# Performance work log

Hardware: AMD Instinct MI355X
Metric: run time of the kernel (lower is better)

## Reference

```python
import jax, jax.numpy as jnp
import numpy as np

N = 40000      # nodes
E = 640000     # edges (avg degree 16)
IN = 128
H = 128
OUT = 64


def setup_inputs() -> dict:
    key = jax.random.key(0)
    ks = jax.random.split(key, 10)
    s_in = 1.0 / np.sqrt(IN)
    s_h = 1.0 / np.sqrt(H)
    return {
        "x": jax.random.normal(ks[0], (N, IN), jnp.float32),
        "edge_index": jax.random.randint(ks[1], (2, E), 0, N, dtype=jnp.int64),
        "W1l": jax.random.normal(ks[2], (IN, H), jnp.float32) * s_in,
        "W1r": jax.random.normal(ks[3], (IN, H), jnp.float32) * s_in,
        "b1": jnp.zeros((H,), jnp.float32),
        "W2l": jax.random.normal(ks[4], (H, H), jnp.float32) * s_h,
        "W2r": jax.random.normal(ks[5], (H, H), jnp.float32) * s_h,
        "b2": jnp.zeros((H,), jnp.float32),
        "Wout": jax.random.normal(ks[6], (H, OUT), jnp.float32) * s_h,
        "bout": jnp.zeros((OUT,), jnp.float32),
    }


def _sage_conv(x, src, dst, Wl, Wr, b):
    # mean aggregation of source features onto destination nodes
    msg = x[src]                                   # [E, d] gather
    agg = jax.ops.segment_sum(msg, dst, num_segments=N)       # [N, d]
    deg = jax.ops.segment_sum(jnp.ones((src.shape[0],), x.dtype), dst,
                              num_segments=N)                  # [N]
    agg = agg / jnp.maximum(deg, 1.0)[:, None]
    # PyG SAGEConv: lin_l(aggregated neighbors) + lin_r(root); bias on lin_l
    return agg @ Wl + x @ Wr + b


def reference(x, edge_index, W1l, W1r, b1, W2l, W2r, b2, Wout, bout):
    src, dst = edge_index[0], edge_index[1]
    h = jax.nn.relu(_sage_conv(x, src, dst, W1l, W1r, b1))
    h = jax.nn.relu(_sage_conv(h, src, dst, W2l, W2r, b2))
    return h @ Wout + bout
```

## Files before the change

### kernel.cpp

```cpp
#include <hip/hip_runtime.h>


typedef __attribute__((ext_vector_type(8))) short short8v;
typedef __attribute__((ext_vector_type(4))) float f32x4;
typedef __attribute__((ext_vector_type(4))) _Float16 half4v;
typedef __attribute__((ext_vector_type(8))) _Float16 half8v;

#define CAP 64

static __device__ __forceinline__ unsigned short f2bf(float f) {
  unsigned u = __float_as_uint(f);
  u += 0x7fffu + ((u >> 16) & 1u);
  return (unsigned short)(u >> 16);
}
static __device__ __forceinline__ float bf2f(unsigned short h) {
  return __uint_as_float(((unsigned)h) << 16);
}

__global__ __launch_bounds__(256) void k_setup(
    const int* __restrict__ src, const int* __restrict__ dst,
    int* __restrict__ cnt, ushort* __restrict__ csr,
    const float* __restrict__ W1l, const float* __restrict__ W1r,
    const float* __restrict__ W2l, const float* __restrict__ W2r,
    ushort* __restrict__ w1h, ushort* __restrict__ w1lo,
    ushort* __restrict__ w2h, ushort* __restrict__ w2lo,
    const float* __restrict__ Wout, ushort* __restrict__ woh,
    ushort* __restrict__ wol, const float* __restrict__ x,
    _Float16* __restrict__ xh, int E, int N) {
  int t = blockIdx.x * 256 + threadIdx.x;
  if (t < E) {
    int d = dst[t];
    int pos = atomicAdd(&cnt[d], 1);
    if (pos < CAP) csr[(size_t)d * CAP + pos] = (ushort)src[t];
    return;
  }
  t -= E;
  if (t < 8192) {
    const bool is2 = t >= 4096;
    int u = t & 4095;
    const float* Wl = is2 ? W2l : W1l;
    const float* Wr = is2 ? W2r : W1r;
    ushort* wh = is2 ? w2h : w1h;
    ushort* wlo = is2 ? w2lo : w1lo;
    int l = u & 63;
    int n = (u >> 6) & 7;
    int s = u >> 9;
    int col = n * 16 + (l & 15);
    int kb = s * 32 + ((l >> 4) * 8);
    size_t base = ((size_t)(s * 8 + n) * 64 + l) * 8;
#pragma unroll
    for (int j = 0; j < 8; ++j) {
      int k = kb + j;
      float w = (k < 128) ? Wl[(size_t)k * 128 + col] : Wr[(size_t)(k - 128) * 128 + col];
      unsigned short hb = f2bf(w);
      wh[base + j] = hb;
      wlo[base + j] = f2bf(w - bf2f(hb));
    }
    return;
  }
  t -= 8192;
  if (t < 1024) {
    int l = t & 63;
    int n = (t >> 6) & 3;
    int s = t >> 8;
    int col = n * 16 + (l & 15);
    int kb = s * 32 + ((l >> 4) * 8);
    size_t base = ((size_t)(s * 4 + n) * 64 + l) * 8;
#pragma unroll
    for (int j = 0; j < 8; ++j) {
      float w = Wout[(size_t)(kb + j) * 64 + col];
      unsigned short hb = f2bf(w);
      woh[base + j] = hb;
      wol[base + j] = f2bf(w - bf2f(hb));
    }
    return;
  }
  t -= 1024;
  if (t < N * 32) {
    float4 v = reinterpret_cast<const float4*>(x)[t];
    half4v o = {(_Float16)v.x, (_Float16)v.y, (_Float16)v.z, (_Float16)v.w};
    reinterpret_cast<half4v*>(xh)[t] = o;
  }
}

__global__ __launch_bounds__(256) void k_agg(const _Float16* __restrict__ feat,
                                             const int* __restrict__ cnt,
                                             const ushort* __restrict__ csr,
                                             _Float16* __restrict__ agg, int N) {
  const int lane = threadIdx.x & 63;
  const int q = lane >> 4;
  const int c = (lane & 15) * 8;
  const int wave = threadIdx.x >> 6;
  const int node0 = blockIdx.x * 16 + wave * 4 + q;
  const bool valid = node0 < N;
  const int node = valid ? node0 : (N - 1);
  const int deg = cnt[node];
  const int stored = deg < CAP ? deg : CAP;
  const ushort* idx = csr + (size_t)node * CAP;
  float a[8] = {};
  for (int j = 0; j < stored; j += 16) {
    half8v v[16];
#pragma unroll
    for (int u = 0; u < 16; ++u) {
      if (j + u < stored) {
        int nb = idx[j + u];
        v[u] = *reinterpret_cast<const half8v*>(feat + (size_t)nb * 128 + c);
      }
    }
#pragma unroll
    for (int t = 0; t < 8; ++t) {
      float s0 = 0.f, s1 = 0.f, s2 = 0.f, s3 = 0.f;
#pragma unroll
      for (int u = 0; u < 16; u += 4) {
        if (j + u + 0 < stored) s0 += (float)v[u + 0][t];
        if (j + u + 1 < stored) s1 += (float)v[u + 1][t];
        if (j + u + 2 < stored) s2 += (float)v[u + 2][t];
        if (j + u + 3 < stored) s3 += (float)v[u + 3][t];
      }
      a[t] += (s0 + s1) + (s2 + s3);
    }
  }
  if (valid) {
    float invd = 1.0f / fmaxf((float)deg, 1.0f);
    half8v o;
#pragma unroll
    for (int t = 0; t < 8; ++t) o[t] = (_Float16)(a[t] * invd);
    *reinterpret_cast<half8v*>(agg + (size_t)node * 128 + c) = o;
  }
}

__global__ __launch_bounds__(256) void k_gemm1(
    const _Float16* __restrict__ aggh, const _Float16* __restrict__ rooth,
    const ushort* __restrict__ wh, const ushort* __restrict__ wl_,
    const float* __restrict__ bias, _Float16* __restrict__ outh, int M) {
  const int lane = threadIdx.x & 63;
  const int wave = threadIdx.x >> 6;
  const int row = blockIdx.x * 64 + wave * 16;
  f32x4 acc[8] = {};

  for (int s = 0; s < 8; ++s) {
    const int kb = (s & 3) * 32;
    const size_t aoff = (size_t)(row + (lane & 15)) * 128 + kb + (lane >> 4) * 8;
    const _Float16* ap = (s < 4) ? (aggh + aoff) : (rooth + aoff);
    half8v hv = *reinterpret_cast<const half8v*>(ap);
    float av[8];
#pragma unroll
    for (int j = 0; j < 8; ++j) av[j] = (float)hv[j];
    short8v ah, al;
#pragma unroll
    for (int j = 0; j < 8; ++j) {
      unsigned short hb = f2bf(av[j]);
      ah[j] = (short)hb;
      al[j] = (short)f2bf(av[j] - bf2f(hb));
    }
    const size_t sbase = (size_t)s * 8 * 64 * 8 + (size_t)lane * 8;
#pragma unroll
    for (int n = 0; n < 8; ++n) {
      short8v bh = *reinterpret_cast<const short8v*>(wh + sbase + (size_t)n * 64 * 8);
      short8v bl = *reinterpret_cast<const short8v*>(wl_ + sbase + (size_t)n * 64 * 8);
      acc[n] = __builtin_amdgcn_mfma_f32_16x16x32_bf16(ah, bh, acc[n], 0, 0, 0);
      acc[n] = __builtin_amdgcn_mfma_f32_16x16x32_bf16(ah, bl, acc[n], 0, 0, 0);
      acc[n] = __builtin_amdgcn_mfma_f32_16x16x32_bf16(al, bh, acc[n], 0, 0, 0);
    }
  }

  const int r0 = row + (lane >> 4) * 4;
  const int col0 = lane & 15;
#pragma unroll
  for (int n = 0; n < 8; ++n) {
    int col = n * 16 + col0;
    float bv = bias[col];
#pragma unroll
    for (int r = 0; r < 4; ++r) {
      float v = fmaxf(acc[n][r] + bv, 0.f);
      outh[(size_t)(r0 + r) * 128 + col] = (_Float16)v;
    }
  }
}

__global__ __launch_bounds__(256) void k_gemm2_out(
    const _Float16* __restrict__ aggh, const _Float16* __restrict__ rooth,
    const ushort* __restrict__ w2h, const ushort* __restrict__ w2l,
    const float* __restrict__ b2, const ushort* __restrict__ woh,
    const ushort* __restrict__ wol, const float* __restrict__ bout,
    float* __restrict__ out, int M) {
  __shared__ float H[64][132];
  const int lane = threadIdx.x & 63;
  const int wave = threadIdx.x >> 6;
  const int row = blockIdx.x * 64 + wave * 16;
  f32x4 acc[8] = {};

  for (int s = 0; s < 8; ++s) {
    const int kb = (s & 3) * 32;
    const size_t aoff = (size_t)(row + (lane & 15)) * 128 + kb + (lane >> 4) * 8;
    const _Float16* ap = (s < 4) ? (aggh + aoff) : (rooth + aoff);
    half8v hv = *reinterpret_cast<const half8v*>(ap);
    float av[8];
#pragma unroll
    for (int j = 0; j < 8; ++j) av[j] = (float)hv[j];
    short8v ah, al;
#pragma unroll
    for (int j = 0; j < 8; ++j) {
      unsigned short hb = f2bf(av[j]);
      ah[j] = (short)hb;
      al[j] = (short)f2bf(av[j] - bf2f(hb));
    }
    const size_t sbase = (size_t)s * 8 * 64 * 8 + (size_t)lane * 8;
#pragma unroll
    for (int n = 0; n < 8; ++n) {
      short8v bh = *reinterpret_cast<const short8v*>(w2h + sbase + (size_t)n * 64 * 8);
      short8v bl = *reinterpret_cast<const short8v*>(w2l + sbase + (size_t)n * 64 * 8);
      acc[n] = __builtin_amdgcn_mfma_f32_16x16x32_bf16(ah, bh, acc[n], 0, 0, 0);
      acc[n] = __builtin_amdgcn_mfma_f32_16x16x32_bf16(ah, bl, acc[n], 0, 0, 0);
      acc[n] = __builtin_amdgcn_mfma_f32_16x16x32_bf16(al, bh, acc[n], 0, 0, 0);
    }
  }

  const int r0loc = wave * 16 + (lane >> 4) * 4;
  const int col0 = lane & 15;
#pragma unroll
  for (int n = 0; n < 8; ++n) {
    int col = n * 16 + col0;
    float bv = b2[col];
#pragma unroll
    for (int r = 0; r < 4; ++r) {
      H[r0loc + r][col] = fmaxf(acc[n][r] + bv, 0.f);
    }
  }
  __syncthreads();

  f32x4 acc2[4] = {};
  for (int s = 0; s < 4; ++s) {
    const float* hp = &H[wave * 16 + (lane & 15)][s * 32 + (lane >> 4) * 8];
    float av[8];
#pragma unroll
    for (int j = 0; j < 8; ++j) av[j] = hp[j];
    short8v ah, al;
#pragma unroll
    for (int j = 0; j < 8; ++j) {
      unsigned short hb = f2bf(av[j]);
      ah[j] = (short)hb;
      al[j] = (short)f2bf(av[j] - bf2f(hb));
    }
    const size_t sbase = (size_t)s * 4 * 64 * 8 + (size_t)lane * 8;
#pragma unroll
    for (int n = 0; n < 4; ++n) {
      short8v bh = *reinterpret_cast<const short8v*>(woh + sbase + (size_t)n * 64 * 8);
      short8v bl = *reinterpret_cast<const short8v*>(wol + sbase + (size_t)n * 64 * 8);
      acc2[n] = __builtin_amdgcn_mfma_f32_16x16x32_bf16(ah, bh, acc2[n], 0, 0, 0);
      acc2[n] = __builtin_amdgcn_mfma_f32_16x16x32_bf16(ah, bl, acc2[n], 0, 0, 0);
      acc2[n] = __builtin_amdgcn_mfma_f32_16x16x32_bf16(al, bh, acc2[n], 0, 0, 0);
    }
  }

  const int r0 = row + (lane >> 4) * 4;
#pragma unroll
  for (int n = 0; n < 4; ++n) {
    int col = n * 16 + col0;
    float bv = bout[col];
#pragma unroll
    for (int r = 0; r < 4; ++r) {
      out[(size_t)(r0 + r) * 64 + col] = acc2[n][r] + bv;
    }
  }
}

extern "C" void kernel_launch(void* const* d_in, const int* in_sizes, int n_in,
                              void* d_out, int out_size, void* d_ws, size_t ws_size,
                              hipStream_t stream) {
  const float* x    = (const float*)d_in[0];
  const int*   ei   = (const int*)d_in[1];
  const float* W1l  = (const float*)d_in[2];
  const float* W1r  = (const float*)d_in[3];
  const float* b1   = (const float*)d_in[4];
  const float* W2l  = (const float*)d_in[5];
  const float* W2r  = (const float*)d_in[6];
  const float* b2   = (const float*)d_in[7];
  const float* Wout = (const float*)d_in[8];
  const float* bout = (const float*)d_in[9];
  float* out = (float*)d_out;

  const int N = in_sizes[0] / 128;
  const int E = in_sizes[1] / 2;
  const int* src = ei;
  const int* dst = ei + E;

  auto align = [](size_t b) { return (b + 255) & ~(size_t)255; };
  char* p = (char*)d_ws;
  int* cnt       = (int*)p;       p += align((size_t)N * 4);
  ushort* csr    = (ushort*)p;    p += align((size_t)N * CAP * 2);
  _Float16* xh   = (_Float16*)p;  p += align((size_t)N * 128 * 2);
  _Float16* h1h  = (_Float16*)p;  p += align((size_t)N * 128 * 2);
  _Float16* aggh = (_Float16*)p;  p += align((size_t)N * 128 * 2);
  ushort* w1h    = (ushort*)p;    p += align(32768 * 2);
  ushort* w1lo   = (ushort*)p;    p += align(32768 * 2);
  ushort* w2h    = (ushort*)p;    p += align(32768 * 2);
  ushort* w2lo   = (ushort*)p;    p += align(32768 * 2);
  ushort* woh    = (ushort*)p;    p += align(8192 * 2);
  ushort* wol    = (ushort*)p;    p += align(8192 * 2);

  (void)hipMemsetAsync(cnt, 0, (size_t)N * 4, stream);

  const int gemmBlocks = (N + 63) / 64;
  const int aggBlocks = (N + 15) / 16;
  const int setupThreads = E + 8192 + 1024 + N * 32;

  k_setup<<<(setupThreads + 255) / 256, 256, 0, stream>>>(
      src, dst, cnt, csr, W1l, W1r, W2l, W2r, w1h, w1lo, w2h, w2lo,
      Wout, woh, wol, x, xh, E, N);

  k_agg<<<aggBlocks, 256, 0, stream>>>(xh, cnt, csr, aggh, N);
  k_gemm1<<<gemmBlocks, 256, 0, stream>>>(aggh, xh, w1h, w1lo, b1, h1h, N);

  k_agg<<<aggBlocks, 256, 0, stream>>>(h1h, cnt, csr, aggh, N);
  k_gemm2_out<<<gemmBlocks, 256, 0, stream>>>(aggh, h1h, w2h, w2lo, b2,
                                              woh, wol, bout, out, N);
}
```

Baseline: 155.5 us.

## Build compact CSR via count, prefix scan, and fill instead of fixed-cap buckets

Replaces the fixed 64-slot per-node neighbor buckets with an exact CSR: the setup kernel only counts in-degrees, then a three-kernel prefix scan builds row pointers and a fill pass scatters source indices with atomics. The aggregation kernel reads from the row pointers and its inner batch shrinks from 16 to 8 neighbors. The aim is to drop the degree cap (a correctness fix for high-degree nodes) and to give denser, contiguous index reads. In exchange it adds four extra launches, including a single-thread serial block scan, and a second pass of atomics over the edges.

```diff
diff --git a/kernel.cpp b/kernel.cpp
--- a/kernel.cpp
+++ b/kernel.cpp
@@ -6,8 +6,6 @@
 typedef __attribute__((ext_vector_type(4))) _Float16 half4v;
 typedef __attribute__((ext_vector_type(8))) _Float16 half8v;
 
-#define CAP 64
-
 static __device__ __forceinline__ unsigned short f2bf(float f) {
   unsigned u = __float_as_uint(f);
   u += 0x7fffu + ((u >> 16) & 1u);
@@ -18,8 +16,7 @@
 }
 
 __global__ __launch_bounds__(256) void k_setup(
-    const int* __restrict__ src, const int* __restrict__ dst,
-    int* __restrict__ cnt, ushort* __restrict__ csr,
+    const int* __restrict__ dst, int* __restrict__ cnt,
     const float* __restrict__ W1l, const float* __restrict__ W1r,
     const float* __restrict__ W2l, const float* __restrict__ W2r,
     ushort* __restrict__ w1h, ushort* __restrict__ w1lo,
@@ -29,9 +26,7 @@
     _Float16* __restrict__ xh, int E, int N) {
   int t = blockIdx.x * 256 + threadIdx.x;
   if (t < E) {
-    int d = dst[t];
-    int pos = atomicAdd(&cnt[d], 1);
-    if (pos < CAP) csr[(size_t)d * CAP + pos] = (ushort)src[t];
+    atomicAdd(&cnt[dst[t]], 1);
     return;
   }
   t -= E;
@@ -83,9 +78,84 @@
   }
 }
 
+__global__ __launch_bounds__(1024) void k_bsum(const int* __restrict__ cnt,
+                                               int* __restrict__ blockSums, int N) {
+  __shared__ int ws[16];
+  int i = blockIdx.x * 1024 + threadIdx.x;
+  int v = (i < N) ? cnt[i] : 0;
+#pragma unroll
+  for (int d = 32; d > 0; d >>= 1) v += __shfl_xor(v, d, 64);
+  if ((threadIdx.x & 63) == 0) ws[threadIdx.x >> 6] = v;
+  __syncthreads();
+  if (threadIdx.x == 0) {
+    int s = 0;
+#pragma unroll
+    for (int w = 0; w < 16; ++w) s += ws[w];
+    blockSums[blockIdx.x] = s;
+  }
+}
+
+__global__ __launch_bounds__(64) void k_bscan(const int* __restrict__ blockSums,
+                                              int* __restrict__ blockOff,
+                                              int* __restrict__ rowptr, int nb, int N) {
+  if (threadIdx.x == 0) {
+    int run = 0;
+    for (int i = 0; i < nb; ++i) {
+      blockOff[i] = run;
+      run += blockSums[i];
+    }
+    rowptr[N] = run;
+  }
+}
+
+__global__ __launch_bounds__(1024) void k_escan(const int* __restrict__ cnt,
+                                                const int* __restrict__ blockOff,
+                                                int* __restrict__ rowptr,
+                                                int* __restrict__ cursor, int N) {
+  __shared__ int warpSums[16];
+  const int tid = threadIdx.x;
+  const int lane = tid & 63, wid = tid >> 6;
+  int i = blockIdx.x * 1024 + tid;
+  int v = (i < N) ? cnt[i] : 0;
+  int s = v;
+#pragma unroll
+  for (int d = 1; d < 64; d <<= 1) {
+    int t = __shfl_up(s, d, 64);
+    if (lane >= d) s += t;
+  }
+  if (lane == 63) warpSums[wid] = s;
+  __syncthreads();
+  if (tid < 16) {
+    int w = warpSums[tid];
+#pragma unroll
+    for (int d = 1; d < 16; d <<= 1) {
+      int t = __shfl_up(w, d, 16);
+      if (tid >= d) w += t;
+    }
+    warpSums[tid] = w;
+  }
+  __syncthreads();
+  int ex = blockOff[blockIdx.x] + (wid ? warpSums[wid - 1] : 0) + s - v;
+  if (i < N) {
+    rowptr[i] = ex;
+    cursor[i] = ex;
+  }
+}
+
+__global__ __launch_bounds__(256) void k_fill(const int* __restrict__ src,
+                                              const int* __restrict__ dst,
+                                              int* __restrict__ cursor,
+                                              ushort* __restrict__ csr_src, int E) {
+  int e = blockIdx.x * 256 + threadIdx.x;
+  if (e < E) {
+    int pos = atomicAdd(&cursor[dst[e]], 1);
+    csr_src[pos] = (ushort)src[e];
+  }
+}
+
 __global__ __launch_bounds__(256) void k_agg(const _Float16* __restrict__ feat,
-                                             const int* __restrict__ cnt,
-                                             const ushort* __restrict__ csr,
+                                             const int* __restrict__ rowptr,
+                                             const ushort* __restrict__ csr_src,
                                              _Float16* __restrict__ agg, int N) {
   const int lane = threadIdx.x & 63;
   const int q = lane >> 4;
@@ -94,30 +164,32 @@
   const int node0 = blockIdx.x * 16 + wave * 4 + q;
   const bool valid = node0 < N;
   const int node = valid ? node0 : (N - 1);
-  const int deg = cnt[node];
-  const int stored = deg < CAP ? deg : CAP;
-  const ushort* idx = csr + (size_t)node * CAP;
+  const int beg = rowptr[node];
+  const int deg = rowptr[node + 1] - beg;
+  const ushort* idx = csr_src + beg;
   float a[8] = {};
-  for (int j = 0; j < stored; j += 16) {
-    half8v v[16];
-#pragma unroll
-    for (int u = 0; u < 16; ++u) {
-      if (j + u < stored) {
-        int nb = idx[j + u];
-        v[u] = *reinterpret_cast<const half8v*>(feat + (size_t)nb * 128 + c);
-      }
-    }
+  for (int j = 0; j < deg; j += 8) {
+    half8v v0, v1, v2, v3, v4, v5, v6, v7;
+    if (j + 0 < deg) { int nb = idx[j + 0]; v0 = *reinterpret_cast<const half8v*>(feat + (size_t)nb * 128 + c); }
+    if (j + 1 < deg) { int nb = idx[j + 1]; v1 = *reinterpret_cast<const half8v*>(feat + (size_t)nb * 128 + c); }
+    if (j + 2 < deg) { int nb = idx[j + 2]; v2 = *reinterpret_cast<const half8v*>(feat + (size_t)nb * 128 + c); }
+    if (j + 3 < deg) { int nb = idx[j + 3]; v3 = *reinterpret_cast<const half8v*>(feat + (size_t)nb * 128 + c); }
+    if (j + 4 < deg) { int nb = idx[j + 4]; v4 = *reinterpret_cast<const half8v*>(feat + (size_t)nb * 128 + c); }
+    if (j + 5 < deg) { int nb = idx[j + 5]; v5 = *reinterpret_cast<const half8v*>(feat + (size_t)nb * 128 + c); }
+    if (j + 6 < deg) { int nb = idx[j + 6]; v6 = *reinterpret_cast<const half8v*>(feat + (size_t)nb * 128 + c); }
+    if (j + 7 < deg) { int nb = idx[j + 7]; v7 = *reinterpret_cast<const half8v*>(feat + (size_t)nb * 128 + c); }
 #pragma unroll
     for (int t = 0; t < 8; ++t) {
-      float s0 = 0.f, s1 = 0.f, s2 = 0.f, s3 = 0.f;
-#pragma unroll
-      for (int u = 0; u < 16; u += 4) {
-        if (j + u + 0 < stored) s0 += (float)v[u + 0][t];
-        if (j + u + 1 < stored) s1 += (float)v[u + 1][t];
-        if (j + u + 2 < stored) s2 += (float)v[u + 2][t];
-        if (j + u + 3 < stored) s3 += (float)v[u + 3][t];
-      }
-      a[t] += (s0 + s1) + (s2 + s3);
+      float s0 = 0.f, s1 = 0.f;
+      if (j + 0 < deg) s0 += (float)v0[t];
+      if (j + 1 < deg) s1 += (float)v1[t];
+      if (j + 2 < deg) s0 += (float)v2[t];
+      if (j + 3 < deg) s1 += (float)v3[t];
+      if (j + 4 < deg) s0 += (float)v4[t];
+      if (j + 5 < deg) s1 += (float)v5[t];
+      if (j + 6 < deg) s0 += (float)v6[t];
+      if (j + 7 < deg) s1 += (float)v7[t];
+      a[t] += s0 + s1;
     }
   }
   if (valid) {
@@ -288,7 +360,11 @@
   auto align = [](size_t b) { return (b + 255) & ~(size_t)255; };
   char* p = (char*)d_ws;
   int* cnt       = (int*)p;       p += align((size_t)N * 4);
-  ushort* csr    = (ushort*)p;    p += align((size_t)N * CAP * 2);
+  int* rowptr    = (int*)p;       p += align((size_t)(N + 1) * 4);
+  int* cursor    = (int*)p;       p += align((size_t)N * 4);
+  int* blockSums = (int*)p;       p += align(64 * 4);
+  int* blockOff  = (int*)p;       p += align(64 * 4);
+  ushort* csr    = (ushort*)p;    p += align((size_t)E * 2);
   _Float16* xh   = (_Float16*)p;  p += align((size_t)N * 128 * 2);
   _Float16* h1h  = (_Float16*)p;  p += align((size_t)N * 128 * 2);
   _Float16* aggh = (_Float16*)p;  p += align((size_t)N * 128 * 2);
@@ -301,18 +377,24 @@
 
   (void)hipMemsetAsync(cnt, 0, (size_t)N * 4, stream);
 
+  const int nb = (N + 1023) / 1024;
   const int gemmBlocks = (N + 63) / 64;
   const int aggBlocks = (N + 15) / 16;
   const int setupThreads = E + 8192 + 1024 + N * 32;
 
   k_setup<<<(setupThreads + 255) / 256, 256, 0, stream>>>(
-      src, dst, cnt, csr, W1l, W1r, W2l, W2r, w1h, w1lo, w2h, w2lo,
+      dst, cnt, W1l, W1r, W2l, W2r, w1h, w1lo, w2h, w2lo,
       Wout, woh, wol, x, xh, E, N);
 
-  k_agg<<<aggBlocks, 256, 0, stream>>>(xh, cnt, csr, aggh, N);
+  k_bsum<<<nb, 1024, 0, stream>>>(cnt, blockSums, N);
+  k_bscan<<<1, 64, 0, stream>>>(blockSums, blockOff, rowptr, nb, N);
+  k_escan<<<nb, 1024, 0, stream>>>(cnt, blockOff, rowptr, cursor, N);
+  k_fill<<<(E + 255) / 256, 256, 0, stream>>>(src, dst, cursor, csr, E);
+
+  k_agg<<<aggBlocks, 256, 0, stream>>>(xh, rowptr, csr, aggh, N);
   k_gemm1<<<gemmBlocks, 256, 0, stream>>>(aggh, xh, w1h, w1lo, b1, h1h, N);
 
-  k_agg<<<aggBlocks, 256, 0, stream>>>(h1h, cnt, csr, aggh, N);
+  k_agg<<<aggBlocks, 256, 0, stream>>>(h1h, rowptr, csr, aggh, N);
   k_gemm2_out<<<gemmBlocks, 256, 0, stream>>>(aggh, h1h, w2h, w2lo, b2,
                                               woh, wol, bout, out, N);
 }
```

Result: slower. 180.5 us (+16.1%).
